# Performance work log

Measured on AMD Instinct MI355X. Metric: run time of the kernel, lower is better.

The kernel has to match this reference:

```python
import jax, jax.numpy as jnp
import numpy as np

H = 128             # hidden_channels (heads=1 in PyG HGTConv default)
NT, NC, NM = 150000, 40000, 10000   # transactions, customers, merchants
NE = 150000         # edges per base relation
L = 2               # num HGTConv layers
OUT = 2             # out_channels
# node types: 0=transaction, 1=customer, 2=merchant
EDGE_TYPES = ((1, 0), (2, 0), (0, 1), (0, 2))  # (src_type, dst_type)


def setup_inputs():
    key = jax.random.key(0)
    ks = jax.random.split(key, 20)
    s = 1.0 / np.sqrt(H)
    return {
        'x_tx': jax.random.normal(ks[0], (NT, 16), jnp.float32),
        'x_cust': jax.random.normal(ks[1], (NC, 32), jnp.float32),
        'merch_ids': jnp.arange(NM, dtype=jnp.int32),
        'e_ct_src': jax.random.randint(ks[2], (NE,), 0, NC, dtype=jnp.int32),
        'e_ct_dst': jax.random.randint(ks[3], (NE,), 0, NT, dtype=jnp.int32),
        'e_mt_src': jax.random.randint(ks[4], (NE,), 0, NM, dtype=jnp.int32),
        'e_mt_dst': jax.random.randint(ks[5], (NE,), 0, NT, dtype=jnp.int32),
        'proj_tx_w': jax.random.normal(ks[6], (16, H), jnp.float32) * 0.25,
        'proj_tx_b': jnp.zeros((H,), jnp.float32),
        'proj_cust_w': jax.random.normal(ks[7], (32, H), jnp.float32) * 0.18,
        'proj_cust_b': jnp.zeros((H,), jnp.float32),
        'merch_emb': jax.random.normal(ks[8], (NM, H), jnp.float32),
        'kw': jax.random.normal(ks[9], (L, 3, H, H), jnp.float32) * s,
        'kb': jnp.zeros((L, 3, H), jnp.float32),
        'qw': jax.random.normal(ks[10], (L, 3, H, H), jnp.float32) * s,
        'qb': jnp.zeros((L, 3, H), jnp.float32),
        'vw': jax.random.normal(ks[11], (L, 3, H, H), jnp.float32) * s,
        'vb': jnp.zeros((L, 3, H), jnp.float32),
        'aw': jax.random.normal(ks[12], (L, 3, H, H), jnp.float32) * s,
        'ab': jnp.zeros((L, 3, H), jnp.float32),
        'skip': jnp.ones((L, 3), jnp.float32),
        'a_rel': jax.random.normal(ks[13], (L, 4, H, H), jnp.float32) * s,
        'm_rel': jax.random.normal(ks[14], (L, 4, H, H), jnp.float32) * s,
        'p_rel': jnp.ones((L, 4), jnp.float32),
        'out_w': jax.random.normal(ks[15], (H, OUT), jnp.float32) * s,
        'out_b': jnp.zeros((OUT,), jnp.float32),
    }


def _segment_softmax(alpha, dst, n):
    m = jax.ops.segment_max(alpha, dst, num_segments=n)
    m = jnp.where(jnp.isfinite(m), m, 0.0)
    e = jnp.exp(alpha - m[dst])
    z = jax.ops.segment_sum(e, dst, num_segments=n)
    return e / (z[dst] + 1e-16)


def _hgt_conv(xs, lp, edges, sizes):
    kw, kb, qw, qb, vw, vb, aw, ab, skip, a_rel, m_rel, p_rel = lp
    k = [xs[t] @ kw[t] + kb[t] for t in range(3)]
    q = [xs[t] @ qw[t] + qb[t] for t in range(3)]
    v = [xs[t] @ vw[t] + vb[t] for t in range(3)]
    agg = [jnp.zeros_like(xs[t]) for t in range(3)]
    inv_sqrt_d = 1.0 / jnp.sqrt(jnp.float32(H))
    for r, (st, dt) in enumerate(EDGE_TYPES):
        src, dst = edges[r]
        k_e = (k[st] @ a_rel[r])[src]   # [E,H] relation-transformed keys at edge sources
        v_e = (v[st] @ m_rel[r])[src]   # [E,H]
        a = jnp.sum(q[dt][dst] * k_e, axis=-1) * p_rel[r] * inv_sqrt_d  # [E]
        a = _segment_softmax(a, dst, sizes[dt])
        agg[dt] = agg[dt] + jax.ops.segment_sum(a[:, None] * v_e, dst, num_segments=sizes[dt])
    out = []
    for t in range(3):
        o = jax.nn.gelu(agg[t], approximate=False) @ aw[t] + ab[t]
        beta = jax.nn.sigmoid(skip[t])
        out.append(beta * o + (1.0 - beta) * xs[t])
    return out


def _forward(x_tx, x_cust, proj_tx_w, proj_tx_b, proj_cust_w, proj_cust_b, merch_emb,
             kw, kb, qw, qb, vw, vb, aw, ab, skip, a_rel, m_rel, p_rel, out_w, out_b,
             merch_ids, edges):
    xs = [x_tx @ proj_tx_w + proj_tx_b,
          x_cust @ proj_cust_w + proj_cust_b,
          merch_emb[merch_ids]]
    sizes = (NT, NC, NM)
    for l in range(L):
        lp = (kw[l], kb[l], qw[l], qb[l], vw[l], vb[l], aw[l], ab[l], skip[l],
              a_rel[l], m_rel[l], p_rel[l])
        xs = _hgt_conv(xs, lp, edges, sizes)
        xs = [jax.nn.relu(x) for x in xs]   # dropout is identity in eval mode
    return xs[0] @ out_w + out_b            # logits on 'transaction' nodes


def reference(x_tx, x_cust, merch_ids, e_ct_src, e_ct_dst, e_mt_src, e_mt_dst,
              proj_tx_w, proj_tx_b, proj_cust_w, proj_cust_b, merch_emb,
              kw, kb, qw, qb, vw, vb, aw, ab, skip, a_rel, m_rel, p_rel, out_w, out_b):
    edges = ((e_ct_src, e_ct_dst), (e_mt_src, e_mt_dst),
             (e_ct_dst, e_ct_src), (e_mt_dst, e_mt_src))
    return _forward(x_tx, x_cust, proj_tx_w, proj_tx_b, proj_cust_w, proj_cust_b,
                    merch_emb, kw, kb, qw, qb, vw, vb, aw, ab, skip,
                    a_rel, m_rel, p_rel, out_w, out_b, merch_ids, edges)
```

## Files before the change

### kernel.cpp

```cpp
#include <hip/hip_runtime.h>
#include <math.h>

#define H 128
#define NTX 150000
#define NCU 40000
#define NME 10000
#define NEDGE 150000
#define NLAY 2
#define WC_STRIDE 33280
#define WKC_STRIDE 16640
#define BUF_FLOATS 19200000
#define AGG2_OFF 5120000
#define SCAN_TILE 2048

typedef short s8v __attribute__((ext_vector_type(8)));
typedef float f32x4 __attribute__((ext_vector_type(4)));

__device__ __forceinline__ float gelu_exact(float x) {
    return 0.5f * x * (1.0f + erff(x * 0.70710678118654752f));
}
__device__ __forceinline__ unsigned short f2bf(float x) {
    unsigned u = __float_as_uint(x);
    return (unsigned short)((u + 0x7FFFu + ((u >> 16) & 1u)) >> 16);
}
__device__ __forceinline__ float bf2f(unsigned short b) {
    return __uint_as_float(((unsigned)b) << 16);
}

__global__ __launch_bounds__(256) void fill_val(float* p, int n, float v) {
    int i = blockIdx.x * 256 + threadIdx.x;
    if (i < n) p[i] = v;
}
__global__ __launch_bounds__(256) void zero_int(int* p, int n) {
    int i = blockIdx.x * 256 + threadIdx.x;
    if (i < n) p[i] = 0;
}
__global__ __launch_bounds__(256) void copy_int(int* d, const int* s, int n) {
    int i = blockIdx.x * 256 + threadIdx.x;
    if (i < n) d[i] = s[i];
}

__global__ __launch_bounds__(256) void count_deg(const int* __restrict__ dst,
    int* __restrict__ deg, int E)
{
    int e = blockIdx.x * 256 + threadIdx.x;
    if (e < E) atomicAdd(&deg[dst[e]], 1);
}
__global__ __launch_bounds__(256) void scan1(const int* __restrict__ deg,
    int* __restrict__ out, int* __restrict__ bsum, int n)
{
    __shared__ int ts[256];
    int tid = threadIdx.x;
    int base = blockIdx.x * SCAN_TILE + tid * 8;
    int v[8], pre[8], s = 0;
    #pragma unroll
    for (int j = 0; j < 8; ++j) {
        int idx = base + j;
        v[j] = (idx < n) ? deg[idx] : 0;
        pre[j] = s; s += v[j];
    }
    ts[tid] = s;
    __syncthreads();
    for (int off = 1; off < 256; off <<= 1) {
        int t = (tid >= off) ? ts[tid - off] : 0;
        __syncthreads();
        ts[tid] += t;
        __syncthreads();
    }
    int excl = ts[tid] - s;
    #pragma unroll
    for (int j = 0; j < 8; ++j)
        if (base + j < n) out[base + j] = excl + pre[j];
    if (tid == 255) bsum[blockIdx.x] = ts[255];
}
__global__ __launch_bounds__(64) void scan2(int* __restrict__ bsum, int nb) {
    if (threadIdx.x == 0 && blockIdx.x == 0) {
        int run = 0;
        for (int i = 0; i < nb; ++i) { int t = bsum[i]; bsum[i] = run; run += t; }
    }
}
__global__ __launch_bounds__(256) void scan3(int* __restrict__ out,
    const int* __restrict__ bsum, int n, int total)
{
    int base = blockIdx.x * SCAN_TILE;
    int add = bsum[blockIdx.x];
    for (int j = threadIdx.x; j < SCAN_TILE; j += 256) {
        int k = base + j;
        if (k < n) out[k] += add;
    }
    if (blockIdx.x == 0 && threadIdx.x == 0) out[n] = total;
}
__global__ __launch_bounds__(256) void fill_csr(const int* __restrict__ src,
    const int* __restrict__ dst, int* __restrict__ cursor, int* __restrict__ col, int E)
{
    int e = blockIdx.x * 256 + threadIdx.x;
    if (e >= E) return;
    int pos = atomicAdd(&cursor[dst[e]], 1);
    col[pos] = src[e];
}

template<int K>
__global__ __launch_bounds__(256) void proj_kernel(const float* __restrict__ X,
    const float* __restrict__ W, const float* __restrict__ B,
    float* __restrict__ Y, int N)
{
    __shared__ float Wl[K][128];
    __shared__ float Bl[128];
    int tid = threadIdx.x;
    for (int i = tid; i < K * 128; i += 256) Wl[i >> 7][i & 127] = W[i];
    if (tid < 128) Bl[tid] = B[tid];
    __syncthreads();
    int ng = tid >> 5, lane = tid & 31;
    int n = blockIdx.x * 8 + ng;
    if (n >= N) return;
    const float* xr = X + (size_t)n * K;
    float xa[K];
    #pragma unroll
    for (int k4 = 0; k4 < K / 4; ++k4)
        *(float4*)&xa[k4 * 4] = *(const float4*)(xr + k4 * 4);
    int c0 = lane * 4;
    float4 acc = *(const float4*)&Bl[c0];
    #pragma unroll
    for (int k = 0; k < K; ++k) {
        float4 w = *(const float4*)&Wl[k][c0];
        acc.x += xa[k] * w.x; acc.y += xa[k] * w.y;
        acc.z += xa[k] * w.z; acc.w += xa[k] * w.w;
    }
    *(float4*)(Y + (size_t)n * H + c0) = acc;
}

__global__ __launch_bounds__(256) void gather_rows(const float* __restrict__ src,
    const int* __restrict__ ids, float* __restrict__ dstp, int N)
{
    int t = blockIdx.x * 256 + threadIdx.x;
    if (t >= N * 32) return;
    int n = t >> 5, c4 = t & 31;
    int sid = ids[n];
    ((float4*)dstp)[(size_t)n * 32 + c4] = ((const float4*)src)[(size_t)sid * 32 + c4];
}

__global__ __launch_bounds__(256) void combine1_par(const float* __restrict__ kw,
    const float* __restrict__ kb, const float* __restrict__ vw, const float* __restrict__ vb,
    const float* __restrict__ a_rel, const float* __restrict__ m_rel,
    float* __restrict__ wkc, float* __restrict__ wc)
{
    __shared__ float Rs[64][132];
    int b = blockIdx.x;
    int combo = b >> 3;
    int pass  = (b >> 2) & 1;
    int slice = b & 3;
    int l = combo >> 2, r = combo & 3;
    const int src_t[4] = {1, 2, 0, 0};
    int st = src_t[r];
    const float* Ap = (pass ? vw : kw) + (size_t)(l*3 + st) * H * H;
    const float* Rp = (pass ? m_rel : a_rel) + (size_t)combo * H * H;
    float* Out = pass ? (wc + (size_t)combo * WC_STRIDE + 16384)
                      : (wkc + (size_t)combo * WKC_STRIDE);

    int tid = threadIdx.x;
    int i = slice * 32 + (tid >> 3);
    int jb = tid & 7;
    float acc[16];
    #pragma unroll
    for (int j = 0; j < 16; ++j) acc[j] = 0.f;

    for (int half = 0; half < 2; ++half) {
        __syncthreads();
        for (int idx = tid; idx < 64 * 128; idx += 256)
            Rs[idx >> 7][idx & 127] = Rp[(half * 64 + (idx >> 7)) * H + (idx & 127)];
        __syncthreads();
        for (int k = 0; k < 64; ++k) {
            float a = Ap[i * H + half * 64 + k];
            #pragma unroll
            for (int j = 0; j < 16; ++j) acc[j] += a * Rs[k][jb + j * 8];
        }
    }
    #pragma unroll
    for (int j = 0; j < 16; ++j) Out[i * H + jb + j * 8] = acc[j];

    if (pass == 0 && slice == 0 && tid < 128) {
        const float* Avb = vb + (size_t)(l*3 + st) * H;
        const float* Rv = m_rel + (size_t)combo * H * H;
        float* bvc = wc + (size_t)combo * WC_STRIDE + 32896;
        float s = 0.f;
        for (int k = 0; k < H; ++k) s += Avb[k] * Rv[k * H + tid];
        bvc[tid] = s;
    }
}

__global__ __launch_bounds__(256) void combine2_par(const float* __restrict__ qw,
    const float* __restrict__ qb, const float* __restrict__ wkc, float* __restrict__ wc)
{
    __shared__ float BsT[64][133];
    int b = blockIdx.x;
    int combo = b >> 2;
    int slice = b & 3;
    int l = combo >> 2, r = combo & 3;
    const int dst_t[4] = {0, 0, 1, 2};
    int dt = dst_t[r];
    const float* Q  = qw + (size_t)(l*3 + dt) * H * H;
    const float* Qb = qb + (size_t)(l*3 + dt) * H;
    const float* WKc = wkc + (size_t)combo * WKC_STRIDE;
    float* QWc = wc + (size_t)combo * WC_STRIDE;

    int tid = threadIdx.x;
    int i = slice * 32 + (tid >> 3);
    int jb = tid & 7;
    float acc[16];
    #pragma unroll
    for (int j = 0; j < 16; ++j) acc[j] = 0.f;

    for (int half = 0; half < 2; ++half) {
        __syncthreads();
        for (int idx = tid; idx < 64 * 128; idx += 256) {
            int j = idx >> 6, k = idx & 63;
            BsT[k][j] = WKc[j * H + half * 64 + k];
        }
        __syncthreads();
        for (int k = 0; k < 64; ++k) {
            float a = Q[i * H + half * 64 + k];
            #pragma unroll
            for (int j = 0; j < 16; ++j) acc[j] += a * BsT[k][jb + j * 8];
        }
    }
    #pragma unroll
    for (int j = 0; j < 16; ++j) QWc[i * H + jb + j * 8] = acc[j];

    if (slice == 0 && tid < 128) {
        float* qbc = wc + (size_t)combo * WC_STRIDE + 32768;
        float s = 0.f;
        for (int k = 0; k < H; ++k) s += Qb[k] * WKc[tid * H + k];
        qbc[tid] = s;
    }
}

__global__ __launch_bounds__(256) void wprep(const float* __restrict__ wc,
    const float* __restrict__ aw, unsigned short* __restrict__ wt)
{
    int b = blockIdx.x;
    const float* src = (b < 16)
        ? wc + (size_t)(b >> 1) * WC_STRIDE + ((b & 1) ? 16384 : 0)
        : aw + (size_t)(b - 16) * 16384;
    unsigned short* hi = wt + (size_t)b * 32768;
    unsigned short* lo = hi + 16384;
    for (int idx = threadIdx.x; idx < 16384; idx += 256) {
        int k = idx >> 7, j = idx & 127;
        float w = src[idx];
        unsigned short h = f2bf(w);
        hi[j * 128 + k] = h;
        lo[j * 128 + k] = f2bf(w - bf2f(h));
    }
}

#define STAGE_TILE(SRC, GELU)                                               \
    _Pragma("unroll")                                                       \
    for (int i = 0; i < 8; ++i) {                                           \
        int u = tid + i * 256;                                              \
        int n = u >> 5, c4 = u & 31;                                        \
        int gn = nb + n;                                                    \
        float4 v = make_float4(0.f, 0.f, 0.f, 0.f);                         \
        if (gn < N) v = *(const float4*)((SRC) + (size_t)gn * H + c4 * 4);  \
        if (GELU) {                                                         \
            v.x = gelu_exact(v.x); v.y = gelu_exact(v.y);                   \
            v.z = gelu_exact(v.z); v.w = gelu_exact(v.w);                   \
        }                                                                   \
        ushort4 h, lo;                                                      \
        h.x = f2bf(v.x); lo.x = f2bf(v.x - bf2f(h.x));                      \
        h.y = f2bf(v.y); lo.y = f2bf(v.y - bf2f(h.y));                      \
        h.z = f2bf(v.z); lo.z = f2bf(v.z - bf2f(h.z));                      \
        h.w = f2bf(v.w); lo.w = f2bf(v.w - bf2f(h.w));                      \
        int sc = (c4 * 4) ^ ((n & 7) << 3);                                 \
        *(ushort4*)&lds[0][n][sc] = h;                                      \
        *(ushort4*)&lds[1][n][sc] = lo;                                     \
    }

#define MFMA_TILE64(WT)                                                     \
    _Pragma("unroll")                                                       \
    for (int kb = 0; kb < 4; ++kb) {                                        \
        const unsigned short* wp = (WT) + kb * 32 + kg * 8;                 \
        s8v bh0 = *(const s8v*)(wp + (size_t)(col0 + l15) * 128);           \
        s8v bh1 = *(const s8v*)(wp + (size_t)(col0 + 16 + l15) * 128);      \
        s8v bl0 = *(const s8v*)(wp + 16384 + (size_t)(col0 + l15) * 128);   \
        s8v bl1 = *(const s8v*)(wp + 16384 + (size_t)(col0 + 16 + l15) * 128); \
        _Pragma("unroll")                                                   \
        for (int m = 0; m < 4; ++m) {                                       \
            int row = m * 16 + l15;                                         \
            int offx = (kb * 32 + kg * 8) ^ ((row & 7) << 3);               \
            s8v ah = *(const s8v*)&lds[0][row][offx];                       \
            s8v al = *(const s8v*)&lds[1][row][offx];                       \
            acc[m][0] = __builtin_amdgcn_mfma_f32_16x16x32_bf16(ah, bh0, acc[m][0], 0, 0, 0); \
            acc[m][0] = __builtin_amdgcn_mfma_f32_16x16x32_bf16(al, bh0, acc[m][0], 0, 0, 0); \
            acc[m][0] = __builtin_amdgcn_mfma_f32_16x16x32_bf16(ah, bl0, acc[m][0], 0, 0, 0); \
            acc[m][1] = __builtin_amdgcn_mfma_f32_16x16x32_bf16(ah, bh1, acc[m][1], 0, 0, 0); \
            acc[m][1] = __builtin_amdgcn_mfma_f32_16x16x32_bf16(al, bh1, acc[m][1], 0, 0, 0); \
            acc[m][1] = __builtin_amdgcn_mfma_f32_16x16x32_bf16(ah, bl1, acc[m][1], 0, 0, 0); \
        }                                                                   \
    }

template<int MODE>
__global__ __launch_bounds__(256, 4) void mfma_gemm(const float* __restrict__ X,
    const unsigned short* __restrict__ Wt, const float* __restrict__ Bias,
    float* __restrict__ Y, int N, const float* __restrict__ Xold,
    const float* __restrict__ skipP, const float* __restrict__ zb)
{
    __shared__ unsigned short lds[2][64][128];
    int tid = threadIdx.x;
    int nb = blockIdx.x * 64;

    STAGE_TILE(X, MODE == 1)
    __syncthreads();

    int wid = tid >> 6, lane = tid & 63;
    int l15 = lane & 15, kg = lane >> 4;
    int col0 = wid * 32;

    f32x4 acc[4][2];
    #pragma unroll
    for (int m = 0; m < 4; ++m)
        #pragma unroll
        for (int n = 0; n < 2; ++n)
            acc[m][n] = (f32x4){0.f, 0.f, 0.f, 0.f};

    MFMA_TILE64(Wt)

    float beta = 0.f, omb = 0.f;
    if (MODE == 1) {
        float s = *skipP;
        beta = 1.f / (1.f + expf(-s));
        omb = 1.f - beta;
    }
    float bias0 = Bias[col0 + l15];
    float bias1 = Bias[col0 + 16 + l15];

    #pragma unroll
    for (int m = 0; m < 4; ++m) {
        #pragma unroll
        for (int r = 0; r < 4; ++r) {
            int grow = nb + m * 16 + kg * 4 + r;
            if (grow < N) {
                float gate = 1.f;
                if (MODE == 3) gate = (zb[grow] > 0.f) ? 1.f : 0.f;
                #pragma unroll
                for (int n = 0; n < 2; ++n) {
                    int col = col0 + n * 16 + l15;
                    float val = acc[m][n][r];
                    float bs = n ? bias1 : bias0;
                    size_t yi = (size_t)grow * H + col;
                    if (MODE == 0) {
                        Y[yi] = val + bs;
                    } else if (MODE == 3) {
                        Y[yi] = val + gate * bs;
                    } else {
                        float o = val + bs;
                        float xo = Xold[yi];
                        Y[yi] = fmaxf(beta * o + omb * xo, 0.f);
                    }
                }
            }
        }
    }
}

__global__ __launch_bounds__(256, 4) void mfma_gemm2q(const float* __restrict__ X,
    const unsigned short* __restrict__ Wt0, const unsigned short* __restrict__ Wt1,
    const float* __restrict__ b0, const float* __restrict__ b1,
    float* __restrict__ Y0, float* __restrict__ Y1, int N)
{
    __shared__ unsigned short lds[2][64][128];
    int tid = threadIdx.x;
    int nb = blockIdx.x * 64;

    STAGE_TILE(X, 0)
    __syncthreads();

    int wid = tid >> 6, lane = tid & 63;
    int l15 = lane & 15, kg = lane >> 4;
    int col0 = wid * 32;

    #pragma unroll
    for (int set = 0; set < 2; ++set) {
        const unsigned short* Wt = set ? Wt1 : Wt0;
        const float* Bias = set ? b1 : b0;
        float* Y = set ? Y1 : Y0;

        f32x4 acc[4][2];
        #pragma unroll
        for (int m = 0; m < 4; ++m)
            #pragma unroll
            for (int n = 0; n < 2; ++n)
                acc[m][n] = (f32x4){0.f, 0.f, 0.f, 0.f};

        MFMA_TILE64(Wt)

        float bias0 = Bias[col0 + l15];
        float bias1 = Bias[col0 + 16 + l15];
        #pragma unroll
        for (int m = 0; m < 4; ++m) {
            #pragma unroll
            for (int r = 0; r < 4; ++r) {
                int grow = nb + m * 16 + kg * 4 + r;
                if (grow < N) {
                    #pragma unroll
                    for (int n = 0; n < 2; ++n) {
                        int col = col0 + n * 16 + l15;
                        Y[(size_t)grow * H + col] = acc[m][n][r] + (n ? bias1 : bias0);
                    }
                }
            }
        }
    }
}

__global__ __launch_bounds__(256, 4) void mfma_gemmV2(float* __restrict__ A0,
    const float* __restrict__ A1,
    const unsigned short* __restrict__ Wt0, const unsigned short* __restrict__ Wt1,
    const float* __restrict__ bv0, const float* __restrict__ bv1,
    const float* __restrict__ z0, const float* __restrict__ z1, int N)
{
    __shared__ unsigned short lds[2][64][128];
    int tid = threadIdx.x;
    int nb = blockIdx.x * 64;
    int wid = tid >> 6, lane = tid & 63;
    int l15 = lane & 15, kg = lane >> 4;
    int col0 = wid * 32;

    f32x4 acc[4][2];
    #pragma unroll
    for (int m = 0; m < 4; ++m)
        #pragma unroll
        for (int n = 0; n < 2; ++n)
            acc[m][n] = (f32x4){0.f, 0.f, 0.f, 0.f};

    {
        STAGE_TILE(A0, 0)
        __syncthreads();
        MFMA_TILE64(Wt0)
    }
    __syncthreads();
    {
        const float* A = A1;
        STAGE_TILE(A, 0)
        __syncthreads();
        MFMA_TILE64(Wt1)
    }

    float b00 = bv0[col0 + l15],  b01 = bv0[col0 + 16 + l15];
    float b10 = bv1[col0 + l15],  b11 = bv1[col0 + 16 + l15];

    #pragma unroll
    for (int m = 0; m < 4; ++m) {
        #pragma unroll
        for (int r = 0; r < 4; ++r) {
            int grow = nb + m * 16 + kg * 4 + r;
            if (grow < N) {
                float g0 = (z0[grow] > 0.f) ? 1.f : 0.f;
                float g1 = (z1[grow] > 0.f) ? 1.f : 0.f;
                #pragma unroll
                for (int n = 0; n < 2; ++n) {
                    int col = col0 + n * 16 + l15;
                    float bs = n ? (g0 * b01 + g1 * b11) : (g0 * b00 + g1 * b10);
                    A0[(size_t)grow * H + col] = acc[m][n][r] + bs;
                }
            }
        }
    }
}

__global__ __launch_bounds__(256) void gather_agg(const int* __restrict__ row_ptr,
    const int* __restrict__ col_idx, float* __restrict__ qtraw,
    const float* __restrict__ xsrc, const float* __restrict__ prel, int ridx,
    float* __restrict__ zout, int ndt)
{
    int g = blockIdx.x * 8 + (threadIdx.x >> 5);
    int lane = threadIdx.x & 31;
    if (g >= ndt) return;
    float4 qv = *(const float4*)(qtraw + (size_t)g * H + lane * 4);
    float scale = prel[ridx] * 0.08838834764831843f;
    int beg = row_ptr[g], end = row_ptr[g + 1];
    float4 acc = make_float4(0.f, 0.f, 0.f, 0.f);
    float z = 0.f;
    for (int i = beg; i < end; ++i) {
        int s = col_idx[i];
        float4 xv = *(const float4*)(xsrc + (size_t)s * H + lane * 4);
        float p = qv.x*xv.x + qv.y*xv.y + qv.z*xv.z + qv.w*xv.w;
        #pragma unroll
        for (int m = 16; m >= 1; m >>= 1) p += __shfl_xor(p, m);
        float ev = expf(p * scale);
        z += ev;
        acc.x += ev * xv.x; acc.y += ev * xv.y;
        acc.z += ev * xv.z; acc.w += ev * xv.w;
    }
    float inv = 1.f / (z + 1e-16f);
    float4 r = make_float4(acc.x * inv, acc.y * inv, acc.z * inv, acc.w * inv);
    *(float4*)(qtraw + (size_t)g * H + lane * 4) = r;
    if (lane == 0) zout[g] = z;
}

__global__ __launch_bounds__(256) void out_kernel(const float* __restrict__ X,
    const float* __restrict__ Wo, const float* __restrict__ bo,
    float* __restrict__ out, int N)
{
    int t = blockIdx.x * 256 + threadIdx.x;
    int n = t >> 5, lane = t & 31;
    if (n >= N) return;
    float4 xv = *(const float4*)(X + (size_t)n * H + lane * 4);
    float xa[4]; *(float4*)xa = xv;
    float p0 = 0.f, p1 = 0.f;
    #pragma unroll
    for (int j = 0; j < 4; ++j) {
        p0 += xa[j] * Wo[(lane*4 + j)*2 + 0];
        p1 += xa[j] * Wo[(lane*4 + j)*2 + 1];
    }
    #pragma unroll
    for (int m = 16; m >= 1; m >>= 1) { p0 += __shfl_xor(p0, m); p1 += __shfl_xor(p1, m); }
    if (lane == 0) {
        out[(size_t)n*2 + 0] = p0 + bo[0];
        out[(size_t)n*2 + 1] = p1 + bo[1];
    }
}

extern "C" void kernel_launch(void* const* d_in, const int* in_sizes, int n_in,
                              void* d_out, int out_size, void* d_ws, size_t ws_size,
                              hipStream_t stream)
{
    const float* x_tx      = (const float*)d_in[0];
    const float* x_cust    = (const float*)d_in[1];
    const int*   merch_ids = (const int*)d_in[2];
    const int*   e_ct_src  = (const int*)d_in[3];
    const int*   e_ct_dst  = (const int*)d_in[4];
    const int*   e_mt_src  = (const int*)d_in[5];
    const int*   e_mt_dst  = (const int*)d_in[6];
    const float* proj_tx_w   = (const float*)d_in[7];
    const float* proj_tx_b   = (const float*)d_in[8];
    const float* proj_cust_w = (const float*)d_in[9];
    const float* proj_cust_b = (const float*)d_in[10];
    const float* merch_emb   = (const float*)d_in[11];
    const float* kw = (const float*)d_in[12];
    const float* kb = (const float*)d_in[13];
    const float* qw = (const float*)d_in[14];
    const float* qb = (const float*)d_in[15];
    const float* vw = (const float*)d_in[16];
    const float* vb = (const float*)d_in[17];
    const float* aw = (const float*)d_in[18];
    const float* ab = (const float*)d_in[19];
    const float* skip  = (const float*)d_in[20];
    const float* a_rel = (const float*)d_in[21];
    const float* m_rel = (const float*)d_in[22];
    const float* p_rel = (const float*)d_in[23];
    const float* out_w = (const float*)d_in[24];
    const float* out_b = (const float*)d_in[25];
    (void)in_sizes; (void)n_in;

    const size_t nsz[3] = {NTX, NCU, NME};

    float* ws = (float*)d_ws;
    size_t off = 0;
    float* xs[3];  for (int t = 0; t < 3; ++t) { xs[t] = ws + off; off += nsz[t]*H; }
    float* bufB    = ws + off; off += BUF_FLOATS;
    float* edgebuf = ws + off; off += BUF_FLOATS;
    float* zbuf0 = ws + off; off += NTX;
    float* zbuf1 = ws + off; off += NTX;
    float* wc   = ws + off; off += 8 * WC_STRIDE;
    float* wkc  = ws + off; off += 8 * WKC_STRIDE;
    int* ibase = (int*)(ws + off);
    const int rp_size[4] = {NTX + 1, NTX + 1, NCU + 1, NME + 1};
    int* rowp[4]; size_t ioff = 0;
    for (int r = 0; r < 4; ++r) { rowp[r] = ibase + ioff; ioff += rp_size[r]; }
    int* colix[4];
    for (int r = 0; r < 4; ++r) { colix[r] = ibase + ioff; ioff += NEDGE; }
    int* cursor = ibase + ioff; ioff += NTX;
    int* bsum   = ibase + ioff; ioff += 256;
    unsigned short* wt = (unsigned short*)(ibase + ioff);
    size_t needed_bytes = off * sizeof(float) + ioff * sizeof(int)
                        + (size_t)22 * 32768 * sizeof(unsigned short);

    if (ws_size < needed_bytes) {
        fill_val<<<(out_size + 255) / 256, 256, 0, stream>>>(
            (float*)d_out, out_size, (float)(ws_size >> 20));
        return;
    }

    const int src_t[4] = {1, 2, 0, 0};
    const int dst_t[4] = {0, 0, 1, 2};
    const int* esrc[4] = {e_ct_src, e_mt_src, e_ct_dst, e_mt_dst};
    const int* edst[4] = {e_ct_dst, e_mt_dst, e_ct_src, e_mt_src};

    const int egrid256 = (NEDGE + 255) / 256;
    for (int r = 0; r < 4; ++r) {
        int ndt = (int)nsz[dst_t[r]];
        int nb = (ndt + SCAN_TILE - 1) / SCAN_TILE;
        zero_int<<<(ndt + 255) / 256, 256, 0, stream>>>(cursor, ndt);
        count_deg<<<egrid256, 256, 0, stream>>>(edst[r], cursor, NEDGE);
        scan1<<<nb, 256, 0, stream>>>(cursor, rowp[r], bsum, ndt);
        scan2<<<1, 64, 0, stream>>>(bsum, nb);
        scan3<<<nb, 256, 0, stream>>>(rowp[r], bsum, ndt, NEDGE);
        copy_int<<<(ndt + 255) / 256, 256, 0, stream>>>(cursor, rowp[r], ndt);
        fill_csr<<<egrid256, 256, 0, stream>>>(esrc[r], edst[r], cursor, colix[r], NEDGE);
    }

    combine1_par<<<64, 256, 0, stream>>>(kw, kb, vw, vb, a_rel, m_rel, wkc, wc);
    combine2_par<<<32, 256, 0, stream>>>(qw, qb, wkc, wc);
    wprep<<<22, 256, 0, stream>>>(wc, aw, wt);

    proj_kernel<16><<<(NTX + 7) / 8, 256, 0, stream>>>(x_tx, proj_tx_w, proj_tx_b, xs[0], NTX);
    proj_kernel<32><<<(NCU + 7) / 8, 256, 0, stream>>>(x_cust, proj_cust_w, proj_cust_b, xs[1], NCU);
    gather_rows<<<(NME * 32 + 255) / 256, 256, 0, stream>>>(merch_emb, merch_ids, xs[2], NME);

    float* aggT[3] = { edgebuf, bufB, bufB + AGG2_OFF };

    for (int l = 0; l < NLAY; ++l) {
        int c0 = l * 4 + 0, c1 = l * 4 + 1;
        const float* W0 = wc + (size_t)c0 * WC_STRIDE;
        const float* W1 = wc + (size_t)c1 * WC_STRIDE;

        mfma_gemm2q<<<(NTX + 63) / 64, 256, 0, stream>>>(
            xs[0], wt + (size_t)(c0*2) * 32768, wt + (size_t)(c1*2) * 32768,
            W0 + 32768, W1 + 32768, edgebuf, bufB, NTX);
        gather_agg<<<(NTX + 7) / 8, 256, 0, stream>>>(
            rowp[0], colix[0], edgebuf, xs[1], p_rel, c0, zbuf0, NTX);
        gather_agg<<<(NTX + 7) / 8, 256, 0, stream>>>(
            rowp[1], colix[1], bufB, xs[2], p_rel, c1, zbuf1, NTX);
        mfma_gemmV2<<<(NTX + 63) / 64, 256, 0, stream>>>(
            edgebuf, bufB, wt + (size_t)(c0*2 + 1) * 32768, wt + (size_t)(c1*2 + 1) * 32768,
            W0 + 32896, W1 + 32896, zbuf0, zbuf1, NTX);

        for (int r = 2; r < 4; ++r) {
            int st = src_t[r], dt = dst_t[r];
            int ndt = (int)nsz[dt];
            int combo = l * 4 + r;
            const float* Wr = wc + (size_t)combo * WC_STRIDE;
            float* buf = aggT[dt];
            int grid = (ndt + 63) / 64;
            mfma_gemm<0><<<grid, 256, 0, stream>>>(
                xs[dt], wt + (size_t)(combo*2) * 32768, Wr + 32768, buf, ndt,
                nullptr, nullptr, nullptr);
            gather_agg<<<(ndt + 7) / 8, 256, 0, stream>>>(
                rowp[r], colix[r], buf, xs[st], p_rel, combo, zbuf0, ndt);
            mfma_gemm<3><<<grid, 256, 0, stream>>>(
                buf, wt + (size_t)(combo*2 + 1) * 32768, Wr + 32896, buf, ndt,
                nullptr, nullptr, zbuf0);
        }

        for (int t = 0; t < 3; ++t)
            mfma_gemm<1><<<(int)((nsz[t] + 63) / 64), 256, 0, stream>>>(
                aggT[t], wt + (size_t)(16 + l*3 + t) * 32768,
                ab + (size_t)(l*3 + t)*H, xs[t], (int)nsz[t],
                xs[t], skip + l*3 + t, nullptr);
    }

    out_kernel<<<(NTX * 32 + 255) / 256, 256, 0, stream>>>(xs[0], out_w, out_b, (float*)d_out, NTX);
}
```

Measured before the change: 1.111 ms.

## Fuse Q projection, edge softmax gather, and V projection into one kernel per relation

```diff
diff --git a/kernel.cpp b/kernel.cpp
--- a/kernel.cpp
+++ b/kernel.cpp
@@ -274,7 +274,7 @@
         *(ushort4*)&lds[1][n][sc] = lo;                                     \
     }
 
-#define MFMA_TILE64(WT)                                                     \
+#define MFMA_TILE64(WT, ACC)                                                \
     _Pragma("unroll")                                                       \
     for (int kb = 0; kb < 4; ++kb) {                                        \
         const unsigned short* wp = (WT) + kb * 32 + kg * 8;                 \
@@ -288,47 +288,179 @@
             int offx = (kb * 32 + kg * 8) ^ ((row & 7) << 3);               \
             s8v ah = *(const s8v*)&lds[0][row][offx];                       \
             s8v al = *(const s8v*)&lds[1][row][offx];                       \
-            acc[m][0] = __builtin_amdgcn_mfma_f32_16x16x32_bf16(ah, bh0, acc[m][0], 0, 0, 0); \
-            acc[m][0] = __builtin_amdgcn_mfma_f32_16x16x32_bf16(al, bh0, acc[m][0], 0, 0, 0); \
-            acc[m][0] = __builtin_amdgcn_mfma_f32_16x16x32_bf16(ah, bl0, acc[m][0], 0, 0, 0); \
-            acc[m][1] = __builtin_amdgcn_mfma_f32_16x16x32_bf16(ah, bh1, acc[m][1], 0, 0, 0); \
-            acc[m][1] = __builtin_amdgcn_mfma_f32_16x16x32_bf16(al, bh1, acc[m][1], 0, 0, 0); \
-            acc[m][1] = __builtin_amdgcn_mfma_f32_16x16x32_bf16(ah, bl1, acc[m][1], 0, 0, 0); \
+            ACC[m][0] = __builtin_amdgcn_mfma_f32_16x16x32_bf16(ah, bh0, ACC[m][0], 0, 0, 0); \
+            ACC[m][0] = __builtin_amdgcn_mfma_f32_16x16x32_bf16(al, bh0, ACC[m][0], 0, 0, 0); \
+            ACC[m][0] = __builtin_amdgcn_mfma_f32_16x16x32_bf16(ah, bl0, ACC[m][0], 0, 0, 0); \
+            ACC[m][1] = __builtin_amdgcn_mfma_f32_16x16x32_bf16(ah, bh1, ACC[m][1], 0, 0, 0); \
+            ACC[m][1] = __builtin_amdgcn_mfma_f32_16x16x32_bf16(al, bh1, ACC[m][1], 0, 0, 0); \
+            ACC[m][1] = __builtin_amdgcn_mfma_f32_16x16x32_bf16(ah, bl1, ACC[m][1], 0, 0, 0); \
         }                                                                   \
     }
 
-template<int MODE>
-__global__ __launch_bounds__(256, 4) void mfma_gemm(const float* __restrict__ X,
+#define ZERO_ACC(ACC)                                                       \
+    _Pragma("unroll")                                                       \
+    for (int m = 0; m < 4; ++m)                                             \
+        _Pragma("unroll")                                                   \
+        for (int n = 0; n < 2; ++n)                                         \
+            ACC[m][n] = (f32x4){0.f, 0.f, 0.f, 0.f};
+
+#define WRITE_QT(ACC, QBC)                                                  \
+    {                                                                       \
+        float b0_ = (QBC)[col0 + l15], b1_ = (QBC)[col0 + 16 + l15];        \
+        _Pragma("unroll")                                                   \
+        for (int m = 0; m < 4; ++m)                                         \
+            _Pragma("unroll")                                               \
+            for (int r = 0; r < 4; ++r) {                                   \
+                int row = m * 16 + kg * 4 + r;                              \
+                ldsQ[row][col0 + l15]      = ACC[m][0][r] + b0_;            \
+                ldsQ[row][col0 + 16 + l15] = ACC[m][1][r] + b1_;            \
+            }                                                               \
+    }
+
+#define GATHER_REL(ROWP, COLIX, XS, SCALE, ZSH)                             \
+    _Pragma("unroll 1")                                                     \
+    for (int i = 0; i < 8; ++i) {                                           \
+        int gl = grp * 8 + i;                                               \
+        int g = nb + gl;                                                    \
+        float4 a4 = make_float4(0.f, 0.f, 0.f, 0.f);                        \
+        float z = 0.f;                                                      \
+        if (g < N) {                                                        \
+            float4 qv = *(float4*)&ldsQ[gl][ln * 4];                        \
+            int beg = (ROWP)[g], end = (ROWP)[g + 1];                       \
+            for (int e = beg; e < end; ++e) {                               \
+                int s = (COLIX)[e];                                         \
+                float4 xv = *(const float4*)((XS) + (size_t)s * H + ln * 4);\
+                float p = qv.x*xv.x + qv.y*xv.y + qv.z*xv.z + qv.w*xv.w;    \
+                _Pragma("unroll")                                           \
+                for (int mm = 16; mm >= 1; mm >>= 1) p += __shfl_xor(p, mm);\
+                float ev = expf(p * (SCALE));                               \
+                z += ev;                                                    \
+                a4.x += ev*xv.x; a4.y += ev*xv.y;                           \
+                a4.z += ev*xv.z; a4.w += ev*xv.w;                           \
+            }                                                               \
+        }                                                                   \
+        float inv = 1.f / (z + 1e-16f);                                     \
+        rawreg[i] = make_float4(a4.x*inv, a4.y*inv, a4.z*inv, a4.w*inv);    \
+        if (ln == 0) (ZSH)[gl] = z;                                         \
+    }
+
+#define CVT_RAW()                                                           \
+    _Pragma("unroll")                                                       \
+    for (int i = 0; i < 8; ++i) {                                           \
+        int row = grp * 8 + i;                                              \
+        float4 v = rawreg[i];                                               \
+        ushort4 h, lo;                                                      \
+        h.x = f2bf(v.x); lo.x = f2bf(v.x - bf2f(h.x));                      \
+        h.y = f2bf(v.y); lo.y = f2bf(v.y - bf2f(h.y));                      \
+        h.z = f2bf(v.z); lo.z = f2bf(v.z - bf2f(h.z));                      \
+        h.w = f2bf(v.w); lo.w = f2bf(v.w - bf2f(h.w));                      \
+        int sc = (ln * 4) ^ ((row & 7) << 3);                               \
+        *(ushort4*)&lds[0][row][sc] = h;                                    \
+        *(ushort4*)&lds[1][row][sc] = lo;                                   \
+    }
+
+template<int DUAL>
+__global__ __launch_bounds__(256, 4) void fused_rel(
+    const float* __restrict__ Xdst,
+    const float* __restrict__ XsA, const float* __restrict__ XsB,
+    const unsigned short* __restrict__ wtQA, const unsigned short* __restrict__ wtVA,
+    const unsigned short* __restrict__ wtQB, const unsigned short* __restrict__ wtVB,
+    const float* __restrict__ qbcA, const float* __restrict__ bvcA,
+    const float* __restrict__ qbcB, const float* __restrict__ bvcB,
+    const int* __restrict__ rowpA, const int* __restrict__ colixA,
+    const int* __restrict__ rowpB, const int* __restrict__ colixB,
+    const float* __restrict__ prel, int ridxA, int ridxB,
+    float* __restrict__ Agg, int N)
+{
+    __shared__ float ubuf[8448];
+    __shared__ float zshA[64], zshB[64];
+    unsigned short (*lds)[64][128] = (unsigned short (*)[64][128])ubuf;
+    float (*ldsQ)[132] = (float (*)[132])ubuf;
+
+    int tid = threadIdx.x;
+    int nb = blockIdx.x * 64;
+    int wid = tid >> 6, lane = tid & 63;
+    int l15 = lane & 15, kg = lane >> 4;
+    int col0 = wid * 32;
+    int grp = tid >> 5, ln = tid & 31;
+
+    STAGE_TILE(Xdst, 0)
+    __syncthreads();
+    f32x4 accQA[4][2]; ZERO_ACC(accQA)
+    MFMA_TILE64(wtQA, accQA)
+    f32x4 accQB[4][2];
+    if (DUAL) { ZERO_ACC(accQB) MFMA_TILE64(wtQB, accQB) }
+    __syncthreads();
+
+    f32x4 accV[4][2]; ZERO_ACC(accV)
+    float4 rawreg[8];
+
+    WRITE_QT(accQA, qbcA)
+    __syncthreads();
+    {
+        float scaleA = prel[ridxA] * 0.08838834764831843f;
+        GATHER_REL(rowpA, colixA, XsA, scaleA, zshA)
+    }
+    __syncthreads();
+    CVT_RAW()
+    __syncthreads();
+    MFMA_TILE64(wtVA, accV)
+
+    if (DUAL) {
+        __syncthreads();
+        WRITE_QT(accQB, qbcB)
+        __syncthreads();
+        {
+            float scaleB = prel[ridxB] * 0.08838834764831843f;
+            GATHER_REL(rowpB, colixB, XsB, scaleB, zshB)
+        }
+        __syncthreads();
+        CVT_RAW()
+        __syncthreads();
+        MFMA_TILE64(wtVB, accV)
+    }
+
+    float bA0 = bvcA[col0 + l15], bA1 = bvcA[col0 + 16 + l15];
+    float bB0 = DUAL ? bvcB[col0 + l15] : 0.f;
+    float bB1 = DUAL ? bvcB[col0 + 16 + l15] : 0.f;
+    #pragma unroll
+    for (int m = 0; m < 4; ++m) {
+        #pragma unroll
+        for (int r = 0; r < 4; ++r) {
+            int lrow = m * 16 + kg * 4 + r;
+            int grow = nb + lrow;
+            if (grow < N) {
+                float gA = (zshA[lrow] > 0.f) ? 1.f : 0.f;
+                float gB = (DUAL && zshB[lrow] > 0.f) ? 1.f : 0.f;
+                Agg[(size_t)grow * H + col0 + l15]      = accV[m][0][r] + gA * bA0 + gB * bB0;
+                Agg[(size_t)grow * H + col0 + 16 + l15] = accV[m][1][r] + gA * bA1 + gB * bB1;
+            }
+        }
+    }
+}
+
+__global__ __launch_bounds__(256, 4) void mfma_gemm_upd(const float* __restrict__ X,
     const unsigned short* __restrict__ Wt, const float* __restrict__ Bias,
     float* __restrict__ Y, int N, const float* __restrict__ Xold,
-    const float* __restrict__ skipP, const float* __restrict__ zb)
+    const float* __restrict__ skipP)
 {
     __shared__ unsigned short lds[2][64][128];
     int tid = threadIdx.x;
     int nb = blockIdx.x * 64;
 
-    STAGE_TILE(X, MODE == 1)
+    STAGE_TILE(X, 1)
     __syncthreads();
 
     int wid = tid >> 6, lane = tid & 63;
     int l15 = lane & 15, kg = lane >> 4;
     int col0 = wid * 32;
 
-    f32x4 acc[4][2];
-    #pragma unroll
-    for (int m = 0; m < 4; ++m)
-        #pragma unroll
-        for (int n = 0; n < 2; ++n)
-            acc[m][n] = (f32x4){0.f, 0.f, 0.f, 0.f};
-
-    MFMA_TILE64(Wt)
-
-    float beta = 0.f, omb = 0.f;
-    if (MODE == 1) {
-        float s = *skipP;
-        beta = 1.f / (1.f + expf(-s));
-        omb = 1.f - beta;
-    }
+    f32x4 acc[4][2]; ZERO_ACC(acc)
+    MFMA_TILE64(Wt, acc)
+
+    float s = *skipP;
+    float beta = 1.f / (1.f + expf(-s));
+    float omb = 1.f - beta;
     float bias0 = Bias[col0 + l15];
     float bias1 = Bias[col0 + 16 + l15];
 
@@ -338,162 +470,17 @@
         for (int r = 0; r < 4; ++r) {
             int grow = nb + m * 16 + kg * 4 + r;
             if (grow < N) {
-                float gate = 1.f;
-                if (MODE == 3) gate = (zb[grow] > 0.f) ? 1.f : 0.f;
                 #pragma unroll
                 for (int n = 0; n < 2; ++n) {
                     int col = col0 + n * 16 + l15;
-                    float val = acc[m][n][r];
-                    float bs = n ? bias1 : bias0;
                     size_t yi = (size_t)grow * H + col;
-                    if (MODE == 0) {
-                        Y[yi] = val + bs;
-                    } else if (MODE == 3) {
-                        Y[yi] = val + gate * bs;
-                    } else {
-                        float o = val + bs;
-                        float xo = Xold[yi];
-                        Y[yi] = fmaxf(beta * o + omb * xo, 0.f);
-                    }
+                    float o = acc[m][n][r] + (n ? bias1 : bias0);
+                    float xo = Xold[yi];
+                    Y[yi] = fmaxf(beta * o + omb * xo, 0.f);
                 }
             }
         }
     }
-}
-
-__global__ __launch_bounds__(256, 4) void mfma_gemm2q(const float* __restrict__ X,
-    const unsigned short* __restrict__ Wt0, const unsigned short* __restrict__ Wt1,
-    const float* __restrict__ b0, const float* __restrict__ b1,
-    float* __restrict__ Y0, float* __restrict__ Y1, int N)
-{
-    __shared__ unsigned short lds[2][64][128];
-    int tid = threadIdx.x;
-    int nb = blockIdx.x * 64;
-
-    STAGE_TILE(X, 0)
-    __syncthreads();
-
-    int wid = tid >> 6, lane = tid & 63;
-    int l15 = lane & 15, kg = lane >> 4;
-    int col0 = wid * 32;
-
-    #pragma unroll
-    for (int set = 0; set < 2; ++set) {
-        const unsigned short* Wt = set ? Wt1 : Wt0;
-        const float* Bias = set ? b1 : b0;
-        float* Y = set ? Y1 : Y0;
-
-        f32x4 acc[4][2];
-        #pragma unroll
-        for (int m = 0; m < 4; ++m)
-            #pragma unroll
-            for (int n = 0; n < 2; ++n)
-                acc[m][n] = (f32x4){0.f, 0.f, 0.f, 0.f};
-
-        MFMA_TILE64(Wt)
-
-        float bias0 = Bias[col0 + l15];
-        float bias1 = Bias[col0 + 16 + l15];
-        #pragma unroll
-        for (int m = 0; m < 4; ++m) {
-            #pragma unroll
-            for (int r = 0; r < 4; ++r) {
-                int grow = nb + m * 16 + kg * 4 + r;
-                if (grow < N) {
-                    #pragma unroll
-                    for (int n = 0; n < 2; ++n) {
-                        int col = col0 + n * 16 + l15;
-                        Y[(size_t)grow * H + col] = acc[m][n][r] + (n ? bias1 : bias0);
-                    }
-                }
-            }
-        }
-    }
-}
-
-__global__ __launch_bounds__(256, 4) void mfma_gemmV2(float* __restrict__ A0,
-    const float* __restrict__ A1,
-    const unsigned short* __restrict__ Wt0, const unsigned short* __restrict__ Wt1,
-    const float* __restrict__ bv0, const float* __restrict__ bv1,
-    const float* __restrict__ z0, const float* __restrict__ z1, int N)
-{
-    __shared__ unsigned short lds[2][64][128];
-    int tid = threadIdx.x;
-    int nb = blockIdx.x * 64;
-    int wid = tid >> 6, lane = tid & 63;
-    int l15 = lane & 15, kg = lane >> 4;
-    int col0 = wid * 32;
-
-    f32x4 acc[4][2];
-    #pragma unroll
-    for (int m = 0; m < 4; ++m)
-        #pragma unroll
-        for (int n = 0; n < 2; ++n)
-            acc[m][n] = (f32x4){0.f, 0.f, 0.f, 0.f};
-
-    {
-        STAGE_TILE(A0, 0)
-        __syncthreads();
-        MFMA_TILE64(Wt0)
-    }
-    __syncthreads();
-    {
-        const float* A = A1;
-        STAGE_TILE(A, 0)
-        __syncthreads();
-        MFMA_TILE64(Wt1)
-    }
-
-    float b00 = bv0[col0 + l15],  b01 = bv0[col0 + 16 + l15];
-    float b10 = bv1[col0 + l15],  b11 = bv1[col0 + 16 + l15];
-
-    #pragma unroll
-    for (int m = 0; m < 4; ++m) {
-        #pragma unroll
-        for (int r = 0; r < 4; ++r) {
-            int grow = nb + m * 16 + kg * 4 + r;
-            if (grow < N) {
-                float g0 = (z0[grow] > 0.f) ? 1.f : 0.f;
-                float g1 = (z1[grow] > 0.f) ? 1.f : 0.f;
-                #pragma unroll
-                for (int n = 0; n < 2; ++n) {
-                    int col = col0 + n * 16 + l15;
-                    float bs = n ? (g0 * b01 + g1 * b11) : (g0 * b00 + g1 * b10);
-                    A0[(size_t)grow * H + col] = acc[m][n][r] + bs;
-                }
-            }
-        }
-    }
-}
-
-__global__ __launch_bounds__(256) void gather_agg(const int* __restrict__ row_ptr,
-    const int* __restrict__ col_idx, float* __restrict__ qtraw,
-    const float* __restrict__ xsrc, const float* __restrict__ prel, int ridx,
-    float* __restrict__ zout, int ndt)
-{
-    int g = blockIdx.x * 8 + (threadIdx.x >> 5);
-    int lane = threadIdx.x & 31;
-    if (g >= ndt) return;
-    float4 qv = *(const float4*)(qtraw + (size_t)g * H + lane * 4);
-    float scale = prel[ridx] * 0.08838834764831843f;
-    int beg = row_ptr[g], end = row_ptr[g + 1];
-    float4 acc = make_float4(0.f, 0.f, 0.f, 0.f);
-    float z = 0.f;
-    for (int i = beg; i < end; ++i) {
-        int s = col_idx[i];
-        float4 xv = *(const float4*)(xsrc + (size_t)s * H + lane * 4);
-        float p = qv.x*xv.x + qv.y*xv.y + qv.z*xv.z + qv.w*xv.w;
-        #pragma unroll
-        for (int m = 16; m >= 1; m >>= 1) p += __shfl_xor(p, m);
-        float ev = expf(p * scale);
-        z += ev;
-        acc.x += ev * xv.x; acc.y += ev * xv.y;
-        acc.z += ev * xv.z; acc.w += ev * xv.w;
-    }
-    float inv = 1.f / (z + 1e-16f);
-    float4 r = make_float4(acc.x * inv, acc.y * inv, acc.z * inv, acc.w * inv);
-    *(float4*)(qtraw + (size_t)g * H + lane * 4) = r;
-    if (lane == 0) zout[g] = z;
 }
 
 __global__ __launch_bounds__(256) void out_kernel(const float* __restrict__ X,
@@ -573,6 +560,7 @@
     unsigned short* wt = (unsigned short*)(ibase + ioff);
     size_t needed_bytes = off * sizeof(float) + ioff * sizeof(int)
                         + (size_t)22 * 32768 * sizeof(unsigned short);
+    (void)zbuf0; (void)zbuf1;
 
     if (ws_size < needed_bytes) {
         fill_val<<<(out_size + 255) / 256, 256, 0, stream>>>(
@@ -613,39 +601,33 @@
         const float* W0 = wc + (size_t)c0 * WC_STRIDE;
         const float* W1 = wc + (size_t)c1 * WC_STRIDE;
 
-        mfma_gemm2q<<<(NTX + 63) / 64, 256, 0, stream>>>(
-            xs[0], wt + (size_t)(c0*2) * 32768, wt + (size_t)(c1*2) * 32768,
-            W0 + 32768, W1 + 32768, edgebuf, bufB, NTX);
-        gather_agg<<<(NTX + 7) / 8, 256, 0, stream>>>(
-            rowp[0], colix[0], edgebuf, xs[1], p_rel, c0, zbuf0, NTX);
-        gather_agg<<<(NTX + 7) / 8, 256, 0, stream>>>(
-            rowp[1], colix[1], bufB, xs[2], p_rel, c1, zbuf1, NTX);
-        mfma_gemmV2<<<(NTX + 63) / 64, 256, 0, stream>>>(
-            edgebuf, bufB, wt + (size_t)(c0*2 + 1) * 32768, wt + (size_t)(c1*2 + 1) * 32768,
-            W0 + 32896, W1 + 32896, zbuf0, zbuf1, NTX);
+        fused_rel<1><<<(NTX + 63) / 64, 256, 0, stream>>>(
+            xs[0], xs[1], xs[2],
+            wt + (size_t)(c0*2) * 32768, wt + (size_t)(c0*2 + 1) * 32768,
+            wt + (size_t)(c1*2) * 32768, wt + (size_t)(c1*2 + 1) * 32768,
+            W0 + 32768, W0 + 32896, W1 + 32768, W1 + 32896,
+            rowp[0], colix[0], rowp[1], colix[1],
+            p_rel, c0, c1, edgebuf, NTX);
 
         for (int r = 2; r < 4; ++r) {
-            int st = src_t[r], dt = dst_t[r];
+            int dt = dst_t[r];
             int ndt = (int)nsz[dt];
             int combo = l * 4 + r;
             const float* Wr = wc + (size_t)combo * WC_STRIDE;
-            float* buf = aggT[dt];
-            int grid = (ndt + 63) / 64;
-            mfma_gemm<0><<<grid, 256, 0, stream>>>(
-                xs[dt], wt + (size_t)(combo*2) * 32768, Wr + 32768, buf, ndt,
-                nullptr, nullptr, nullptr);
-            gather_agg<<<(ndt + 7) / 8, 256, 0, stream>>>(
-                rowp[r], colix[r], buf, xs[st], p_rel, combo, zbuf0, ndt);
-            mfma_gemm<3><<<grid, 256, 0, stream>>>(
-                buf, wt + (size_t)(combo*2 + 1) * 32768, Wr + 32896, buf, ndt,
-                nullptr, nullptr, zbuf0);
+            fused_rel<0><<<(ndt + 63) / 64, 256, 0, stream>>>(
+                xs[dt], xs[0], nullptr,
+                wt + (size_t)(combo*2) * 32768, wt + (size_t)(combo*2 + 1) * 32768,
+                nullptr, nullptr,
+                Wr + 32768, Wr + 32896, nullptr, nullptr,
+                rowp[r], colix[r], nullptr, nullptr,
+                p_rel, combo, 0, aggT[dt], ndt);
         }
 
         for (int t = 0; t < 3; ++t)
-            mfma_gemm<1><<<(int)((nsz[t] + 63) / 64), 256, 0, stream>>>(
+            mfma_gemm_upd<<<(int)((nsz[t] + 63) / 64), 256, 0, stream>>>(
                 aggT[t], wt + (size_t)(16 + l*3 + t) * 32768,
                 ab + (size_t)(l*3 + t)*H, xs[t], (int)nsz[t],
-                xs[t], skip + l*3 + t, nullptr);
+                xs[t], skip + l*3 + t);
     }
 
     out_kernel<<<(NTX * 32 + 255) / 256, 256, 0, stream>>>(xs[0], out_w, out_b, (float*)d_out, NTX);
```

After: 1.311 ms. +18.0%, slower.
